# Kernel tuning notes

Hardware: AMD Instinct MI355X
Metric: run time of the kernel (lower is better)

The kernel has to match this reference:

```python
import jax, jax.numpy as jnp
import numpy as np

N, E, U, DEPTH = 50000, 800000, 64, 4
NODE_F, EDGE_F = 2, 1
EPS = 1e-5


def setup_inputs() -> dict:
    key = jax.random.key(0)
    ks = jax.random.split(key, 20)
    s = lambda k, shape, fan_in: jax.random.normal(k, shape, jnp.float32) * (1.0 / np.sqrt(fan_in))
    inp = {
        "x": jax.random.normal(ks[0], (N, NODE_F), jnp.float32),
        "edge_index": jax.random.randint(ks[1], (2, E), 0, N, jnp.int32),
        "edge_attr": jax.random.uniform(ks[2], (E, EDGE_F), jnp.float32),
        # input projections
        "node_W": s(ks[3], (NODE_F, U), NODE_F),
        "node_b": jnp.zeros((U,), jnp.float32),
        "edge_W": s(ks[4], (EDGE_F, U), EDGE_F),
        "edge_b": jnp.zeros((U,), jnp.float32),
        # per-layer message MLP: Linear(2U->U), SiLU, Linear(U->U)
        "msg_W1": s(ks[5], (DEPTH, 2 * U, U), 2 * U),
        "msg_b1": jnp.zeros((DEPTH, U), jnp.float32),
        "msg_W2": s(ks[6], (DEPTH, U, U), U),
        "msg_b2": jnp.zeros((DEPTH, U), jnp.float32),
        # per-layer update MLP: Linear(2U->U), SiLU, Linear(U->U)
        "upd_W1": s(ks[7], (DEPTH, 2 * U, U), 2 * U),
        "upd_b1": jnp.zeros((DEPTH, U), jnp.float32),
        "upd_W2": s(ks[8], (DEPTH, U, U), U),
        "upd_b2": jnp.zeros((DEPTH, U), jnp.float32),
        # per-layer LayerNorm
        "ln_g": jnp.ones((DEPTH, U), jnp.float32),
        "ln_b": jnp.zeros((DEPTH, U), jnp.float32),
    }
    return inp


def reference(x, edge_index, edge_attr, node_W, node_b, edge_W, edge_b,
              msg_W1, msg_b1, msg_W2, msg_b2,
              upd_W1, upd_b1, upd_W2, upd_b2, ln_g, ln_b):
    silu = jax.nn.silu
    n = x.shape[0]
    src = edge_index[0]  # x_j (source, gathered)
    dst = edge_index[1]  # aggregation target i

    h = silu(x @ node_W + node_b)           # (n, U)
    e = silu(edge_attr @ edge_W + edge_b)   # (E, U)

    # mean aggregation denominator (in-degree, clamped to 1 as PyG does)
    deg = jax.ops.segment_sum(jnp.ones((src.shape[0],), h.dtype), dst, num_segments=n)
    deg = jnp.maximum(deg, 1.0)[:, None]

    for i in range(DEPTH):
        # message: msg_mlp(cat[x_j, edge_attr])
        m = jnp.concatenate([h[src], e], axis=-1)               # (E, 2U)
        m = silu(m @ msg_W1[i] + msg_b1[i]) @ msg_W2[i] + msg_b2[i]  # (E, U)
        # aggregate: mean over incoming edges
        aggr = jax.ops.segment_sum(m, dst, num_segments=n) / deg     # (n, U)
        # update: update_mlp(cat[x, aggr_out])
        u = jnp.concatenate([h, aggr], axis=-1)                 # (n, 2U)
        h_new = silu(u @ upd_W1[i] + upd_b1[i]) @ upd_W2[i] + upd_b2[i]
        # residual + LayerNorm
        h = h + h_new
        mu = jnp.mean(h, axis=-1, keepdims=True)
        var = jnp.mean(jnp.square(h - mu), axis=-1, keepdims=True)
        h = (h - mu) * jax.lax.rsqrt(var + EPS) * ln_g[i] + ln_b[i]
    return h
```

## Files before the change

### kernel.cpp

```cpp
#include <hip/hip_runtime.h>
#include <hip/hip_fp16.h>

#define NN 50000
#define NE 800000
#define DEPTH 4
#define EPSF 1e-5f
#define GTAB 8192
#define GROWS (GTAB + 1)
#define NWAVE 8192
#define NBKT 196
#define BK_BLOCKS 256
#define EPB (NE / BK_BLOCKS)
#define CSR_MAXE 8192

typedef _Float16 f16;
typedef _Float16 f16x2 __attribute__((ext_vector_type(2)));
typedef _Float16 f16x8 __attribute__((ext_vector_type(8)));
typedef float f32x4 __attribute__((ext_vector_type(4)));

#define MFMA16(a, b, c) __builtin_amdgcn_mfma_f32_16x16x32_f16(a, b, c, 0, 0, 0)

static __device__ __forceinline__ float silu_f(float x) {
    float e = __builtin_amdgcn_exp2f(x * -1.44269504088896f);
    return x * __builtin_amdgcn_rcpf(1.0f + e);
}

#define WT_TOTAL (2 * DEPTH * (8192 + 4096))
#define NB_P0 ((WT_TOTAL + NN * 64 + 255) / 256)
#define NB_GT ((DEPTH * GROWS + 3) / 4)
#define NB_BH BK_BLOCKS
#define NB_PREP (NB_P0 + NB_GT + NB_BH)

__global__ void k_prep(const float* __restrict__ mW1, const float* __restrict__ mW2,
                       const float* __restrict__ uW1, const float* __restrict__ uW2,
                       f16* __restrict__ w1t, f16* __restrict__ w2t,
                       f16* __restrict__ u1t, f16* __restrict__ u2t,
                       const float* __restrict__ x, const float* __restrict__ nW,
                       const float* __restrict__ nb, f16* __restrict__ h16,
                       const float* __restrict__ eW, const float* __restrict__ eb,
                       const float* __restrict__ mb1, f16* __restrict__ G,
                       const int* __restrict__ ei, int* __restrict__ ghist) {
    __shared__ int hist[NBKT];
    __shared__ float es[4][64];
    int blk = blockIdx.x;
    int tid = threadIdx.x;

    if (blk < NB_P0) {
        int i = blk * 256 + tid;
        const int A = DEPTH * 8192, B = DEPTH * 4096;
        if (i < WT_TOTAL) {
            const float* src; f16* dst; int K, rel;
            if (i < A)              { src = mW1; dst = w1t; K = 128; rel = i; }
            else if (i < A + B)     { src = mW2; dst = w2t; K = 64;  rel = i - A; }
            else if (i < 2 * A + B) { src = uW1; dst = u1t; K = 128; rel = i - A - B; }
            else                    { src = uW2; dst = u2t; K = 64;  rel = i - 2 * A - B; }
            int kc = K * 64;
            int d = rel / kc, r = rel - d * kc;
            int k = r / 64, c = r - k * 64;
            dst[d * kc + c * K + k] = (f16)src[rel];
        } else {
            int j = i - WT_TOTAL;
            if (j < NN * 64) {
                int n = j >> 6, u = j & 63;
                h16[j] = (f16)silu_f(fmaf(x[2 * n], nW[u],
                                          fmaf(x[2 * n + 1], nW[64 + u], nb[u])));
            }
        }
    } else if (blk < NB_P0 + NB_GT) {
        int w = tid >> 6, lane = tid & 63;
        int rowid = (blk - NB_P0) * 4 + w;
        if (rowid < DEPTH * GROWS) {
            int l = rowid / GROWS, i = rowid - l * GROWS;
            float xv = (float)i * (1.0f / GTAB);
            es[w][lane] = silu_f(fmaf(xv, eW[lane], eb[lane]));
            float s = mb1[l * 64 + lane];
            const float* Wl = mW1 + (size_t)l * 8192;
            #pragma unroll 8
            for (int u = 0; u < 64; ++u)
                s = fmaf(es[w][u], Wl[(64 + u) * 64 + lane], s);
            G[(size_t)rowid * 64 + lane] = (f16)s;
        }
    } else {
        int b = blk - NB_P0 - NB_GT;
        for (int i = tid; i < NBKT; i += 256) hist[i] = 0;
        __syncthreads();
        int base = b * EPB;
        for (int it = 0; it < EPB; it += 256) {
            if (it + tid < EPB) atomicAdd(&hist[ei[NE + base + it + tid] >> 8], 1);
        }
        __syncthreads();
        for (int bb = tid; bb < NBKT; bb += 256)
            ghist[bb * BK_BLOCKS + b] = hist[bb];
    }
}

__global__ __launch_bounds__(256)
void k_bscan1(int* __restrict__ ghist, int* __restrict__ tot) {
    int tid = threadIdx.x, lane = tid & 63, w = tid >> 6;
    int b = blockIdx.x * 4 + w;
    if (b >= NBKT) return;
    int carry = 0;
    #pragma unroll
    for (int c = 0; c < 4; ++c) {
        int idx = b * BK_BLOCKS + c * 64 + lane;
        int v = ghist[idx];
        int incl = v;
        #pragma unroll
        for (int off = 1; off < 64; off <<= 1) {
            int t = __shfl_up(incl, off, 64);
            if (lane >= off) incl += t;
        }
        ghist[idx] = incl - v + carry;
        carry += __shfl(incl, 63, 64);
    }
    if (lane == 0) tot[b] = carry;
}

__global__ void k_bscan2(const int* __restrict__ tot, int* __restrict__ bstart) {
    int tid = threadIdx.x;
    if (tid >= 64) return;
    int carry = 0;
    #pragma unroll
    for (int c = 0; c < 4; ++c) {
        int i = c * 64 + tid;
        int v = (i < NBKT) ? tot[i] : 0;
        int incl = v;
        #pragma unroll
        for (int off = 1; off < 64; off <<= 1) {
            int t = __shfl_up(incl, off, 64);
            if (tid >= off) incl += t;
        }
        if (i < NBKT) bstart[i] = incl - v + carry;
        carry += __shfl(incl, 63, 64);
    }
    if (tid == 0) bstart[NBKT] = carry;
}

__global__ __launch_bounds__(256)
void k_bscatter(const int* __restrict__ ei, const float* __restrict__ ea,
                const int* __restrict__ goff, const int* __restrict__ bstart,
                unsigned long long* __restrict__ btmp) {
    __shared__ int hist[NBKT], lbase[NBKT], cur[NBKT], gbase[NBKT];
    __shared__ unsigned long long stg[EPB];
    int tid = threadIdx.x;
    for (int i = tid; i < NBKT; i += 256) hist[i] = 0;
    __syncthreads();
    int base = blockIdx.x * EPB;
    for (int it = 0; it < EPB; it += 256) {
        if (it + tid < EPB) atomicAdd(&hist[ei[NE + base + it + tid] >> 8], 1);
    }
    __syncthreads();
    if (tid == 0) {
        int run = 0;
        for (int b = 0; b < NBKT; ++b) { lbase[b] = run; cur[b] = run; run += hist[b]; }
    }
    __syncthreads();
    if (tid < NBKT) gbase[tid] = goff[tid * BK_BLOCKS + blockIdx.x] + bstart[tid];
    __syncthreads();
    for (int it = 0; it < EPB; it += 256) {
        if (it + tid < EPB) {
            int j = base + it + tid;
            int d = ei[NE + j];
            int src = ei[j];
            int gi = (int)fmaf(ea[j], (float)GTAB, 0.5f);
            gi = gi > GTAB ? GTAB : gi;
            unsigned long long e = ((unsigned long long)(unsigned int)d << 32)
                                 | ((unsigned long long)(((unsigned int)gi << 16) | (unsigned int)src));
            int p = atomicAdd(&cur[d >> 8], 1);
            stg[p] = e;
        }
    }
    __syncthreads();
    for (int i = tid; i < EPB; i += 256) {
        unsigned long long e = stg[i];
        int b = (int)(e >> 40);
        btmp[gbase[b] + (i - lbase[b])] = e;
    }
}

__global__ __launch_bounds__(1024)
void k_csr(const unsigned long long* __restrict__ btmp, const int* __restrict__ bstart,
           int* __restrict__ rowptr, unsigned int* __restrict__ epack) {
    __shared__ int hist[256], sbase[256], cur[256];
    __shared__ unsigned int stg[CSR_MAXE];
    int tid = threadIdx.x;
    int b = blockIdx.x;
    int e0 = bstart[b], e1 = bstart[b + 1];
    int ne = e1 - e0;
    int n0 = b << 8;
    int nn = NN - n0; if (nn > 256) nn = 256;
    if (tid < 256) hist[tid] = 0;
    __syncthreads();
    for (int i = tid; i < ne; i += 1024)
        atomicAdd(&hist[(int)(btmp[e0 + i] >> 32) - n0], 1);
    __syncthreads();
    if (tid == 0) {
        int run = e0;
        for (int i = 0; i < 256; ++i) { sbase[i] = run; cur[i] = run - e0; run += hist[i]; }
    }
    __syncthreads();
    if (tid < nn) rowptr[n0 + tid] = sbase[tid];
    if (b == NBKT - 1 && tid == 0) rowptr[NN] = NE;
    bool fits = (ne <= CSR_MAXE);
    for (int i = tid; i < ne; i += 1024) {
        unsigned long long e = btmp[e0 + i];
        int local = (int)(e >> 32) - n0;
        int p = atomicAdd(&cur[local], 1);
        if (fits) stg[p] = (unsigned int)e;
        else epack[e0 + p] = (unsigned int)e;
    }
    __syncthreads();
    if (fits)
        for (int i = tid; i < ne; i += 1024) epack[e0 + i] = stg[i];
}

__global__ void k_wstart(const int* __restrict__ rowptr, int* __restrict__ wstart) {
    int w = blockIdx.x * 256 + threadIdx.x;
    if (w > NWAVE) return;
    int target = (int)(((long long)w * NE) / NWAVE);
    int lo = 0, hi = NN;
    while (lo < hi) {
        int mid = (lo + hi) >> 1;
        if (rowptr[mid] >= target) hi = mid; else lo = mid + 1;
    }
    wstart[w] = lo;
}

#define HP_TILES 3125
#define HP_BLOCKS 391

__global__ __launch_bounds__(512, 4)
void k_hprime(const f16* __restrict__ h16, const f16* __restrict__ w1t,
              f16* __restrict__ hp16) {
    __shared__ f16 wa[64 * 64];
    int tid = threadIdx.x;
    {
        int g = tid;
        int c = g >> 3, k0 = (g & 7) << 3;
        f16x8 v = *(const f16x8*)&w1t[c * 128 + k0];
        *(f16x8*)&wa[(c << 6) | (k0 ^ ((c & 7) << 3))] = v;
    }
    __syncthreads();

    int w = tid >> 6, lane = tid & 63;
    int row = lane & 15, g4 = lane >> 4;

    int tile = blockIdx.x * 8 + w;
    if (tile >= HP_TILES) return;
    int n0 = tile * 16;
    int nA = n0 + row;

    f16x8 ha0 = *(const f16x8*)&h16[(size_t)nA * 64 + g4 * 8];
    f16x8 ha1 = *(const f16x8*)&h16[(size_t)nA * 64 + 32 + g4 * 8];

    int nC = n0 + g4 * 4;
    #pragma unroll
    for (int cb = 0; cb < 4; ++cb) {
        int c = row + 16 * cb;
        f32x4 acc = (f32x4){0.f, 0.f, 0.f, 0.f};
        f16x8 wb0 = *(const f16x8*)&wa[(c << 6) | ((g4 * 8) ^ ((c & 7) << 3))];
        f16x8 wb1 = *(const f16x8*)&wa[(c << 6) | ((32 + g4 * 8) ^ ((c & 7) << 3))];
        acc = MFMA16(ha0, wb0, acc);
        acc = MFMA16(ha1, wb1, acc);
        #pragma unroll
        for (int v = 0; v < 4; ++v)
            hp16[(size_t)(nC + v) * 64 + c] = (f16)acc[v];
    }
}

#define EK_BLOCKS (NWAVE / 4)

__global__ __launch_bounds__(256, 8)
void k_edge(const int* __restrict__ rowptr, const int* __restrict__ wstart,
            const unsigned int* __restrict__ epack,
            const f16* __restrict__ hp16, const f16* __restrict__ G0,
            f16* __restrict__ Sm) {
    int tid = threadIdx.x;
    int w = tid >> 6, lane = tid & 63;
    int half = lane >> 5;
    int c2 = (lane & 31) << 1;

    const f16* hpb = hp16 + c2;
    const f16* gb  = G0 + c2;

    int gw = blockIdx.x * 4 + w;
    int nbeg = wstart[gw], nend = wstart[gw + 1];
    if (nbeg >= nend) return;

    int ke = rowptr[nbeg];
    for (int n = nbeg; n < nend; ++n) {
        int kb0 = ke;
        ke = rowptr[n + 1];
        if (ke <= kb0) continue;
        float acc0 = 0.f, acc1 = 0.f;
        int p = kb0;

        if (p & 1) {
            unsigned int k = epack[p];
            unsigned int hv2 = *(const unsigned int*)(hpb + ((size_t)(k & 0xFFFFu) << 6));
            unsigned int gv2 = *(const unsigned int*)(gb + ((size_t)(k >> 16) << 6));
            f16x2 v = __builtin_bit_cast(f16x2, hv2) + __builtin_bit_cast(f16x2, gv2);
            float s0 = silu_f((float)v[0]);
            float s1 = silu_f((float)v[1]);
            if (!half) { acc0 += s0; acc1 += s1; }
            ++p;
        }

        #pragma unroll 4
        for (; p + 2 <= ke; p += 2) {
            unsigned long long e2 = *(const unsigned long long*)&epack[p];
            unsigned int k = half ? (unsigned int)(e2 >> 32) : (unsigned int)e2;
            unsigned int hv2 = *(const unsigned int*)(hpb + ((size_t)(k & 0xFFFFu) << 6));
            unsigned int gv2 = *(const unsigned int*)(gb + ((size_t)(k >> 16) << 6));
            f16x2 v = __builtin_bit_cast(f16x2, hv2) + __builtin_bit_cast(f16x2, gv2);
            acc0 += silu_f((float)v[0]);
            acc1 += silu_f((float)v[1]);
        }

        if (p < ke) {
            unsigned int k = epack[p];
            unsigned int hv2 = *(const unsigned int*)(hpb + ((size_t)(k & 0xFFFFu) << 6));
            unsigned int gv2 = *(const unsigned int*)(gb + ((size_t)(k >> 16) << 6));
            f16x2 v = __builtin_bit_cast(f16x2, hv2) + __builtin_bit_cast(f16x2, gv2);
            float s0 = silu_f((float)v[0]);
            float s1 = silu_f((float)v[1]);
            if (!half) { acc0 += s0; acc1 += s1; }
        }

        acc0 += __shfl_xor(acc0, 32, 64);
        acc1 += __shfl_xor(acc1, 32, 64);

        float rd = __builtin_amdgcn_rcpf((float)(ke - kb0));
        f16x2 mv;
        mv[0] = (f16)(acc0 * rd);
        mv[1] = (f16)(acc1 * rd);
        if (!half)
            *(unsigned int*)&Sm[(size_t)n * 64 + c2] = __builtin_bit_cast(unsigned int, mv);
    }
}

#define NK_TILES 3125
#define NK_BLOCKS 391

__global__ __launch_bounds__(512, 6)
void k_node(const f16* __restrict__ h16, const f16* __restrict__ Sm,
            const int* __restrict__ rowptr,
            const f16* __restrict__ w2t, const float* __restrict__ b2,
            const f16* __restrict__ u1t, const float* __restrict__ b1u,
            const f16* __restrict__ u2t, const float* __restrict__ b2u,
            const float* __restrict__ lng, const float* __restrict__ lnb,
            const f16* __restrict__ w1an,
            f16* __restrict__ h16o, f16* __restrict__ hp16o,
            float* __restrict__ out32) {
    __shared__ f16 u1s[64 * 128];
    __shared__ f16 w2s[64 * 64], u2s[64 * 64];
    __shared__ float b2s[64], b1us[64], b2us[64], lngs[64], lnbs[64];
    __shared__ f16 trs[8][16 * 64];

    int tid = threadIdx.x;
    {
        const f16x8* u1v = (const f16x8*)u1t;
        #pragma unroll
        for (int it = 0; it < 2; ++it) {
            int g = tid + it * 512;
            int c = g >> 4, k0 = (g & 15) << 3;
            *(f16x8*)&u1s[(c << 7) | (k0 ^ ((c & 7) << 3))] = u1v[g];
        }
        const f16x8* w2v = (const f16x8*)w2t;
        const f16x8* u2v = (const f16x8*)u2t;
        {
            int g = tid;
            int c = g >> 3, k0 = (g & 7) << 3;
            int pp = (c << 6) | (k0 ^ ((c & 7) << 3));
            *(f16x8*)&w2s[pp] = w2v[g];
            *(f16x8*)&u2s[pp] = u2v[g];
        }
    }
    if (tid < 64) {
        b2s[tid] = b2[tid]; b1us[tid] = b1u[tid]; b2us[tid] = b2u[tid];
        lngs[tid] = lng[tid]; lnbs[tid] = lnb[tid];
    }
    __syncthreads();

    int w = tid >> 6, lane = tid & 63;
    int row = lane & 15, g4 = lane >> 4;
    f16* tp = trs[w];

    int tile = blockIdx.x * 8 + w;
    if (tile >= NK_TILES) return;
    int n0 = tile * 16;
    int nA = n0 + row;

    int degA = rowptr[nA + 1] - rowptr[nA];
    f16x8 sa0 = *(const f16x8*)&Sm[(size_t)nA * 64 + g4 * 8];
    f16x8 sa1 = *(const f16x8*)&Sm[(size_t)nA * 64 + 32 + g4 * 8];
    if (degA <= 0) {
        #pragma unroll
        for (int j = 0; j < 8; ++j) { sa0[j] = (f16)0.f; sa1[j] = (f16)0.f; }
    }
    int nC = n0 + g4 * 4;
    int r0 = rowptr[nC], r1 = rowptr[nC + 1], r2 = rowptr[nC + 2],
        r3 = rowptr[nC + 3], r4 = rowptr[nC + 4];
    float f0 = r1 > r0 ? 1.f : 0.f;
    float f1 = r2 > r1 ? 1.f : 0.f;
    float f2 = r3 > r2 ? 1.f : 0.f;
    float f3 = r4 > r3 ? 1.f : 0.f;

    f32x4 agg[4];
    #pragma unroll
    for (int cb = 0; cb < 4; ++cb) {
        int c = row + 16 * cb;
        float bv = b2s[c];
        agg[cb] = (f32x4){bv * f0, bv * f1, bv * f2, bv * f3};
        f16x8 wb0 = *(const f16x8*)&w2s[(c << 6) | ((g4 * 8) ^ ((c & 7) << 3))];
        f16x8 wb1 = *(const f16x8*)&w2s[(c << 6) | ((32 + g4 * 8) ^ ((c & 7) << 3))];
        agg[cb] = MFMA16(sa0, wb0, agg[cb]);
        agg[cb] = MFMA16(sa1, wb1, agg[cb]);
    }

    #pragma unroll
    for (int cb = 0; cb < 4; ++cb) {
        int c = row + 16 * cb;
        #pragma unroll
        for (int v = 0; v < 4; ++v) {
            int r = g4 * 4 + v;
            tp[(r << 6) | (c ^ ((r & 7) << 3))] = (f16)agg[cb][v];
        }
    }
    f16x8 ha0 = *(const f16x8*)&h16[(size_t)nA * 64 + g4 * 8];
    f16x8 ha1 = *(const f16x8*)&h16[(size_t)nA * 64 + 32 + g4 * 8];
    f16x8 aa2 = *(const f16x8*)&tp[(row << 6) | ((g4 * 8) ^ ((row & 7) << 3))];
    f16x8 aa3 = *(const f16x8*)&tp[(row << 6) | ((32 + g4 * 8) ^ ((row & 7) << 3))];

    f32x4 hid[4];
    #pragma unroll
    for (int cb = 0; cb < 4; ++cb) {
        int c = row + 16 * cb;
        float bv = b1us[c];
        hid[cb] = (f32x4){bv, bv, bv, bv};
        hid[cb] = MFMA16(ha0, *(const f16x8*)&u1s[(c << 7) | ((g4 * 8) ^ ((c & 7) << 3))], hid[cb]);
        hid[cb] = MFMA16(ha1, *(const f16x8*)&u1s[(c << 7) | ((32 + g4 * 8) ^ ((c & 7) << 3))], hid[cb]);
        hid[cb] = MFMA16(aa2, *(const f16x8*)&u1s[(c << 7) | ((64 + g4 * 8) ^ ((c & 7) << 3))], hid[cb]);
        hid[cb] = MFMA16(aa3, *(const f16x8*)&u1s[(c << 7) | ((96 + g4 * 8) ^ ((c & 7) << 3))], hid[cb]);
    }

    #pragma unroll
    for (int cb = 0; cb < 4; ++cb) {
        int c = row + 16 * cb;
        #pragma unroll
        for (int v = 0; v < 4; ++v) {
            int r = g4 * 4 + v;
            tp[(r << 6) | (c ^ ((r & 7) << 3))] = (f16)silu_f(hid[cb][v]);
        }
    }
    f16x8 za0 = *(const f16x8*)&tp[(row << 6) | ((g4 * 8) ^ ((row & 7) << 3))];
    f16x8 za1 = *(const f16x8*)&tp[(row << 6) | ((32 + g4 * 8) ^ ((row & 7) << 3))];

    f32x4 out[4];
    #pragma unroll
    for (int cb = 0; cb < 4; ++cb) {
        int c = row + 16 * cb;
        float bv = b2us[c];
        out[cb] = (f32x4){bv, bv, bv, bv};
        out[cb] = MFMA16(za0, *(const f16x8*)&u2s[(c << 6) | ((g4 * 8) ^ ((c & 7) << 3))], out[cb]);
        out[cb] = MFMA16(za1, *(const f16x8*)&u2s[(c << 6) | ((32 + g4 * 8) ^ ((c & 7) << 3))], out[cb]);
    }

    #pragma unroll
    for (int v = 0; v < 4; ++v) {
        int n = nC + v;
        float hp[4];
        float s = 0.f, q = 0.f;
        #pragma unroll
        for (int cb = 0; cb < 4; ++cb) {
            float xv = (float)h16[(size_t)n * 64 + row + 16 * cb] + out[cb][v];
            hp[cb] = xv; s += xv; q += xv * xv;
        }
        #pragma unroll
        for (int off = 1; off < 16; off <<= 1) {
            s += __shfl_xor(s, off, 64);
            q += __shfl_xor(q, off, 64);
        }
        float mu = s * 0.015625f;
        float var = q * 0.015625f - mu * mu;
        float rstd = __builtin_amdgcn_rsqf(var + EPSF);
        int r = g4 * 4 + v;
        #pragma unroll
        for (int cb = 0; cb < 4; ++cb) {
            int c = row + 16 * cb;
            float o = (hp[cb] - mu) * rstd * lngs[c] + lnbs[c];
            if (out32) out32[(size_t)n * 64 + c] = o;
            f16 o16 = (f16)o;
            if (h16o) h16o[(size_t)n * 64 + c] = o16;
            tp[(r << 6) | (c ^ ((r & 7) << 3))] = o16;
        }
    }

    if (w1an) {
        f16x8 pa0 = *(const f16x8*)&tp[(row << 6) | ((g4 * 8) ^ ((row & 7) << 3))];
        f16x8 pa1 = *(const f16x8*)&tp[(row << 6) | ((32 + g4 * 8) ^ ((row & 7) << 3))];
        #pragma unroll
        for (int cb = 0; cb < 4; ++cb) {
            int c = row + 16 * cb;
            f32x4 acc = (f32x4){0.f, 0.f, 0.f, 0.f};
            f16x8 wb0 = *(const f16x8*)&w1an[c * 128 + g4 * 8];
            f16x8 wb1 = *(const f16x8*)&w1an[c * 128 + 32 + g4 * 8];
            acc = MFMA16(pa0, wb0, acc);
            acc = MFMA16(pa1, wb1, acc);
            #pragma unroll
            for (int v = 0; v < 4; ++v)
                hp16o[(size_t)(nC + v) * 64 + c] = (f16)acc[v];
        }
    }
}

extern "C" void kernel_launch(void* const* d_in, const int* in_sizes, int n_in,
                              void* d_out, int out_size, void* d_ws, size_t ws_size,
                              hipStream_t stream) {
    const float* x   = (const float*)d_in[0];
    const int*   ei  = (const int*)d_in[1];
    const float* ea  = (const float*)d_in[2];
    const float* nW  = (const float*)d_in[3];
    const float* nb  = (const float*)d_in[4];
    const float* eW  = (const float*)d_in[5];
    const float* eb  = (const float*)d_in[6];
    const float* mW1 = (const float*)d_in[7];
    const float* mb1 = (const float*)d_in[8];
    const float* mW2 = (const float*)d_in[9];
    const float* mb2 = (const float*)d_in[10];
    const float* uW1 = (const float*)d_in[11];
    const float* ub1 = (const float*)d_in[12];
    const float* uW2 = (const float*)d_in[13];
    const float* ub2 = (const float*)d_in[14];
    const float* lng = (const float*)d_in[15];
    const float* lnb = (const float*)d_in[16];

    char* p = (char*)d_ws;
    f16*   Sm     = (f16*)p;    p += (size_t)NN * 64 * 2;
    f16*   h16    = (f16*)p;    p += (size_t)NN * 64 * 2;
    f16*   hp16   = (f16*)p;    p += (size_t)NN * 64 * 2;
    int*   rowptr = (int*)p;    p += (size_t)(NN + 4) * 4;
    int*   ghist  = (int*)p;    p += (size_t)NBKT * BK_BLOCKS * 4;
    int*   tot    = (int*)p;    p += (size_t)(NBKT + 4) * 4;
    int*   bstart = (int*)p;    p += (size_t)(NBKT + 4) * 4;
    int*   wstart = (int*)p;    p += (size_t)(NWAVE + 4) * 4;
    unsigned int* epack = (unsigned int*)p; p += (size_t)NE * 4;
    unsigned long long* btmp = (unsigned long long*)p; p += (size_t)NE * 8;
    f16*   G      = (f16*)p;    p += (size_t)DEPTH * GROWS * 64 * 2;
    f16*   w1t = (f16*)p;    p += (size_t)DEPTH * 8192 * 2;
    f16*   w2t = (f16*)p;    p += (size_t)DEPTH * 4096 * 2;
    f16*   u1t = (f16*)p;    p += (size_t)DEPTH * 8192 * 2;
    f16*   u2t = (f16*)p;    p += (size_t)DEPTH * 4096 * 2;

    k_prep<<<NB_PREP, 256, 0, stream>>>(mW1, mW2, uW1, uW2, w1t, w2t, u1t, u2t,
                                        x, nW, nb, h16, eW, eb, mb1, G, ei, ghist);
    k_bscan1<<<(NBKT + 3) / 4, 256, 0, stream>>>(ghist, tot);
    k_bscan2<<<1, 64, 0, stream>>>(tot, bstart);
    k_bscatter<<<BK_BLOCKS, 256, 0, stream>>>(ei, ea, ghist, bstart, btmp);
    k_csr<<<NBKT, 1024, 0, stream>>>(btmp, bstart, rowptr, epack);
    k_wstart<<<(NWAVE + 256) / 256, 256, 0, stream>>>(rowptr, wstart);
    k_hprime<<<HP_BLOCKS, 512, 0, stream>>>(h16, w1t, hp16);

    for (int l = 0; l < DEPTH; ++l) {
        bool last = (l == DEPTH - 1);
        k_edge<<<EK_BLOCKS, 256, 0, stream>>>(rowptr, wstart, epack, hp16,
            G + (size_t)l * GROWS * 64, Sm);
        k_node<<<NK_BLOCKS, 512, 0, stream>>>(h16, Sm, rowptr,
            w2t + (size_t)l * 4096, mb2 + l * 64,
            u1t + (size_t)l * 8192, ub1 + l * 64,
            u2t + (size_t)l * 4096, ub2 + l * 64,
            lng + l * 64, lnb + l * 64,
            last ? (const f16*)nullptr : (w1t + (size_t)(l + 1) * 8192),
            last ? (f16*)nullptr : h16, hp16,
            last ? (float*)d_out : (float*)nullptr);
    }
}
```

Baseline: 265.5 us.

## Split gather tables into channel halves and run edge kernel in two passes

```diff
diff --git a/kernel.cpp b/kernel.cpp
--- a/kernel.cpp
+++ b/kernel.cpp
@@ -14,7 +14,6 @@
 #define CSR_MAXE 8192
 
 typedef _Float16 f16;
-typedef _Float16 f16x2 __attribute__((ext_vector_type(2)));
 typedef _Float16 f16x8 __attribute__((ext_vector_type(8)));
 typedef float f32x4 __attribute__((ext_vector_type(4)));
 
@@ -78,7 +77,7 @@
             #pragma unroll 8
             for (int u = 0; u < 64; ++u)
                 s = fmaf(es[w][u], Wl[(64 + u) * 64 + lane], s);
-            G[(size_t)rowid * 64 + lane] = (f16)s;
+            G[((size_t)(l * 2 + (lane >> 5)) * GROWS + i) * 32 + (lane & 31)] = (f16)s;
         }
     } else {
         int b = blk - NB_P0 - NB_GT;
@@ -231,7 +230,7 @@
 
 __global__ __launch_bounds__(512, 4)
 void k_hprime(const f16* __restrict__ h16, const f16* __restrict__ w1t,
-              f16* __restrict__ hp16) {
+              f16* __restrict__ hpA, f16* __restrict__ hpB) {
     __shared__ f16 wa[64 * 64];
     int tid = threadIdx.x;
     {
@@ -262,28 +261,32 @@
         f16x8 wb1 = *(const f16x8*)&wa[(c << 6) | ((32 + g4 * 8) ^ ((c & 7) << 3))];
         acc = MFMA16(ha0, wb0, acc);
         acc = MFMA16(ha1, wb1, acc);
+        f16* dsth = (cb < 2) ? hpA : hpB;
         #pragma unroll
         for (int v = 0; v < 4; ++v)
-            hp16[(size_t)(nC + v) * 64 + c] = (f16)acc[v];
-    }
-}
-
-#define EK_BLOCKS (NWAVE / 4)
+            dsth[(size_t)(nC + v) * 32 + (c & 31)] = (f16)acc[v];
+    }
+}
+
+#define EK_BLOCKS 2048
 
 __global__ __launch_bounds__(256, 8)
 void k_edge(const int* __restrict__ rowptr, const int* __restrict__ wstart,
             const unsigned int* __restrict__ epack,
-            const f16* __restrict__ hp16, const f16* __restrict__ G0,
+            const f16* __restrict__ hpA, const f16* __restrict__ hpB,
+            const f16* __restrict__ GA, const f16* __restrict__ GB,
             f16* __restrict__ Sm) {
     int tid = threadIdx.x;
     int w = tid >> 6, lane = tid & 63;
-    int half = lane >> 5;
-    int c2 = (lane & 31) << 1;
-
-    const f16* hpb = hp16 + c2;
-    const f16* gb  = G0 + c2;
-
-    int gw = blockIdx.x * 4 + w;
+    int pass = blockIdx.x >> 11;
+    int bid = blockIdx.x & 2047;
+    int he = lane >> 5;
+    int ch = lane & 31;
+
+    const f16* hp = (pass ? hpB : hpA) + ch;
+    const f16* gb = (pass ? GB : GA) + ch;
+
+    int gw = bid * 4 + w;
     int nbeg = wstart[gw], nend = wstart[gw + 1];
     if (nbeg >= nend) return;
 
@@ -292,50 +295,40 @@
         int kb0 = ke;
         ke = rowptr[n + 1];
         if (ke <= kb0) continue;
-        float acc0 = 0.f, acc1 = 0.f;
+        float acc = 0.f;
         int p = kb0;
 
         if (p & 1) {
             unsigned int k = epack[p];
-            unsigned int hv2 = *(const unsigned int*)(hpb + ((size_t)(k & 0xFFFFu) << 6));
-            unsigned int gv2 = *(const unsigned int*)(gb + ((size_t)(k >> 16) << 6));
-            f16x2 v = __builtin_bit_cast(f16x2, hv2) + __builtin_bit_cast(f16x2, gv2);
-            float s0 = silu_f((float)v[0]);
-            float s1 = silu_f((float)v[1]);
-            if (!half) { acc0 += s0; acc1 += s1; }
+            float hv = (float)hp[(size_t)(k & 0xFFFFu) << 5];
+            float gv = (float)gb[(size_t)(k >> 16) << 5];
+            float s = silu_f(hv + gv);
+            if (!he) acc += s;
             ++p;
         }
 
         #pragma unroll 4
         for (; p + 2 <= ke; p += 2) {
             unsigned long long e2 = *(const unsigned long long*)&epack[p];
-            unsigned int k = half ? (unsigned int)(e2 >> 32) : (unsigned int)e2;
-            unsigned int hv2 = *(const unsigned int*)(hpb + ((size_t)(k & 0xFFFFu) << 6));
-            unsigned int gv2 = *(const unsigned int*)(gb + ((size_t)(k >> 16) << 6));
-            f16x2 v = __builtin_bit_cast(f16x2, hv2) + __builtin_bit_cast(f16x2, gv2);
-            acc0 += silu_f((float)v[0]);
-            acc1 += silu_f((float)v[1]);
+            unsigned int k = he ? (unsigned int)(e2 >> 32) : (unsigned int)e2;
+            float hv = (float)hp[(size_t)(k & 0xFFFFu) << 5];
+            float gv = (float)gb[(size_t)(k >> 16) << 5];
+            acc += silu_f(hv + gv);
         }
 
         if (p < ke) {
             unsigned int k = epack[p];
-            unsigned int hv2 = *(const unsigned int*)(hpb + ((size_t)(k & 0xFFFFu) << 6));
-            unsigned int gv2 = *(const unsigned int*)(gb + ((size_t)(k >> 16) << 6));
-            f16x2 v = __builtin_bit_cast(f16x2, hv2) + __builtin_bit_cast(f16x2, gv2);
-            float s0 = silu_f((float)v[0]);
-            float s1 = silu_f((float)v[1]);
-            if (!half) { acc0 += s0; acc1 += s1; }
-        }
-
-        acc0 += __shfl_xor(acc0, 32, 64);
-        acc1 += __shfl_xor(acc1, 32, 64);
-
-        float rd = __builtin_amdgcn_rcpf((float)(ke - kb0));
-        f16x2 mv;
-        mv[0] = (f16)(acc0 * rd);
-        mv[1] = (f16)(acc1 * rd);
-        if (!half)
-            *(unsigned int*)&Sm[(size_t)n * 64 + c2] = __builtin_bit_cast(unsigned int, mv);
+            float hv = (float)hp[(size_t)(k & 0xFFFFu) << 5];
+            float gv = (float)gb[(size_t)(k >> 16) << 5];
+            float s = silu_f(hv + gv);
+            if (!he) acc += s;
+        }
+
+        acc += __shfl_xor(acc, 32, 64);
+        if (!he) {
+            float rd = __builtin_amdgcn_rcpf((float)(ke - kb0));
+            Sm[(size_t)n * 64 + pass * 32 + ch] = (f16)(acc * rd);
+        }
     }
 }
 
@@ -350,7 +343,7 @@
             const f16* __restrict__ u2t, const float* __restrict__ b2u,
             const float* __restrict__ lng, const float* __restrict__ lnb,
             const f16* __restrict__ w1an,
-            f16* __restrict__ h16o, f16* __restrict__ hp16o,
+            f16* __restrict__ h16o, f16* __restrict__ hpAo, f16* __restrict__ hpBo,
             float* __restrict__ out32) {
     __shared__ f16 u1s[64 * 128];
     __shared__ f16 w2s[64 * 64], u2s[64 * 64];
@@ -507,9 +500,10 @@
             f16x8 wb1 = *(const f16x8*)&w1an[c * 128 + 32 + g4 * 8];
             acc = MFMA16(pa0, wb0, acc);
             acc = MFMA16(pa1, wb1, acc);
+            f16* dsth = (cb < 2) ? hpAo : hpBo;
             #pragma unroll
             for (int v = 0; v < 4; ++v)
-                hp16o[(size_t)(nC + v) * 64 + c] = (f16)acc[v];
+                dsth[(size_t)(nC + v) * 32 + (c & 31)] = (f16)acc[v];
         }
     }
 }
@@ -538,7 +532,8 @@
     char* p = (char*)d_ws;
     f16*   Sm     = (f16*)p;    p += (size_t)NN * 64 * 2;
     f16*   h16    = (f16*)p;    p += (size_t)NN * 64 * 2;
-    f16*   hp16   = (f16*)p;    p += (size_t)NN * 64 * 2;
+    f16*   hpA    = (f16*)p;    p += (size_t)NN * 32 * 2;
+    f16*   hpB    = (f16*)p;    p += (size_t)NN * 32 * 2;
     int*   rowptr = (int*)p;    p += (size_t)(NN + 4) * 4;
     int*   ghist  = (int*)p;    p += (size_t)NBKT * BK_BLOCKS * 4;
     int*   tot    = (int*)p;    p += (size_t)(NBKT + 4) * 4;
@@ -546,7 +541,7 @@
     int*   wstart = (int*)p;    p += (size_t)(NWAVE + 4) * 4;
     unsigned int* epack = (unsigned int*)p; p += (size_t)NE * 4;
     unsigned long long* btmp = (unsigned long long*)p; p += (size_t)NE * 8;
-    f16*   G      = (f16*)p;    p += (size_t)DEPTH * GROWS * 64 * 2;
+    f16*   G      = (f16*)p;    p += (size_t)DEPTH * 2 * GROWS * 32 * 2;
     f16*   w1t = (f16*)p;    p += (size_t)DEPTH * 8192 * 2;
     f16*   w2t = (f16*)p;    p += (size_t)DEPTH * 4096 * 2;
     f16*   u1t = (f16*)p;    p += (size_t)DEPTH * 8192 * 2;
@@ -559,19 +554,21 @@
     k_bscatter<<<BK_BLOCKS, 256, 0, stream>>>(ei, ea, ghist, bstart, btmp);
     k_csr<<<NBKT, 1024, 0, stream>>>(btmp, bstart, rowptr, epack);
     k_wstart<<<(NWAVE + 256) / 256, 256, 0, stream>>>(rowptr, wstart);
-    k_hprime<<<HP_BLOCKS, 512, 0, stream>>>(h16, w1t, hp16);
+    k_hprime<<<HP_BLOCKS, 512, 0, stream>>>(h16, w1t, hpA, hpB);
 
     for (int l = 0; l < DEPTH; ++l) {
         bool last = (l == DEPTH - 1);
-        k_edge<<<EK_BLOCKS, 256, 0, stream>>>(rowptr, wstart, epack, hp16,
-            G + (size_t)l * GROWS * 64, Sm);
+        const f16* GA = G + (size_t)(l * 2 + 0) * GROWS * 32;
+        const f16* GB = G + (size_t)(l * 2 + 1) * GROWS * 32;
+        k_edge<<<2 * EK_BLOCKS, 256, 0, stream>>>(rowptr, wstart, epack,
+            hpA, hpB, GA, GB, Sm);
         k_node<<<NK_BLOCKS, 512, 0, stream>>>(h16, Sm, rowptr,
             w2t + (size_t)l * 4096, mb2 + l * 64,
             u1t + (size_t)l * 8192, ub1 + l * 64,
             u2t + (size_t)l * 4096, ub2 + l * 64,
             lng + l * 64, lnb + l * 64,
             last ? (const f16*)nullptr : (w1t + (size_t)(l + 1) * 8192),
-            last ? (f16*)nullptr : h16, hp16,
+            last ? (f16*)nullptr : h16, hpA, hpB,
             last ? (float*)d_out : (float*)nullptr);
     }
 }
```

After: 340.0 us. 1.28x slower.
